# Kernel tuning notes

Hardware: AMD Instinct MI355X
Metric: run time of the kernel (lower is better)

The kernel has to match this reference:

```python
import jax, jax.numpy as jnp
import numpy as np

EPS = 1e-5
GROUPS = 32


def setup_inputs() -> dict:
    key = jax.random.key(0)
    ks = jax.random.split(key, 12)
    b, c, h, w = 8, 256, 64, 64
    s = 1.0 / np.sqrt(c)
    return {
        "x": jax.random.normal(ks[0], (b, c, h, w), jnp.float32),
        "gn_w": jax.random.uniform(ks[1], (c,), jnp.float32, 0.5, 1.5),
        "gn_b": jax.random.normal(ks[2], (c,), jnp.float32) * 0.1,
        "wq": jax.random.normal(ks[3], (c, c), jnp.float32) * s,
        "bq": jax.random.normal(ks[4], (c,), jnp.float32) * 0.02,
        "wk": jax.random.normal(ks[5], (c, c), jnp.float32) * s,
        "bk": jax.random.normal(ks[6], (c,), jnp.float32) * 0.02,
        "wv": jax.random.normal(ks[7], (c, c), jnp.float32) * s,
        "bv": jax.random.normal(ks[8], (c,), jnp.float32) * 0.02,
        "wp": jax.random.normal(ks[9], (c, c), jnp.float32) * s,
        "bp": jax.random.normal(ks[10], (c,), jnp.float32) * 0.02,
        "gamma": jax.random.normal(ks[11], (1,), jnp.float32),
    }


def _group_norm(x, weight, bias):
    b, c, h, w = x.shape
    g = min(c, GROUPS)
    xg = x.reshape(b, g, c // g, h * w)
    mean = xg.mean(axis=(2, 3), keepdims=True)
    var = jnp.var(xg, axis=(2, 3), keepdims=True)
    xn = (xg - mean) * jax.lax.rsqrt(var + EPS)
    xn = xn.reshape(b, c, h, w)
    return xn * weight[None, :, None, None] + bias[None, :, None, None]


def reference(x, gn_w, gn_b, wq, bq, wk, bk, wv, bv, wp, bp, gamma):
    b, c, h, w = x.shape
    x_dash = _group_norm(x, gn_w, gn_b)           # (b,c,h,w)
    xf = x_dash.reshape(b, c, h * w)              # (b,c,n)
    # 1x1 convs == per-pixel linear maps over channels
    q = jnp.einsum('oc,bcn->bon', wq, xf) + bq[None, :, None]
    k = jnp.einsum('oc,bcn->bon', wk, xf) + bk[None, :, None]
    v = jnp.einsum('oc,bcn->bon', wv, xf) + bv[None, :, None]
    # attn[b,i,j] = <q[:,i], k[:,j]> / sqrt(c)
    attn = jnp.einsum('bci,bcj->bij', q, k) / jnp.sqrt(jnp.asarray(c, x.dtype))
    attn = jax.nn.softmax(attn, axis=-1)
    # out[b,c,i] = sum_j v[b,c,j] * attn[b,i,j]
    out = jnp.einsum('bcj,bij->bci', v, attn)
    out = jnp.einsum('oc,bcn->bon', wp, out) + bp[None, :, None]
    out = out.reshape(b, c, h, w)
    return x + gamma[0] * out
```

## Files before the change

kernel.cpp:

```cpp
#include <hip/hip_runtime.h>
#include <cstdint>
#include <cstddef>


#define NB   8
#define NC   256
#define NPIX 4096
#define CPG  8

typedef __attribute__((ext_vector_type(8))) short bf16x8;
typedef __attribute__((ext_vector_type(4))) short s16x4;
typedef __attribute__((ext_vector_type(8))) short s16x8;
typedef __attribute__((ext_vector_type(4))) float f32x4;

__device__ __forceinline__ short f2bf(float f) {
  union { float f; uint32_t u; } v; v.f = f;
  return (short)((v.u + 0x7fffu + ((v.u >> 16) & 1u)) >> 16);
}

__device__ __forceinline__ float bf2f(short s) {
  union { uint32_t u; float f; } v;
  v.u = ((uint32_t)(unsigned short)s) << 16;
  return v.f;
}

__device__ __forceinline__ uint32_t cvtpk_bf(float a, float b) {
  uint32_t r;
  asm("v_cvt_pk_bf16_f32 %0, %1, %2" : "=v"(r) : "v"(a), "v"(b));
  return r;
}

__device__ __forceinline__ f32x4 mfma16(bf16x8 a, bf16x8 b, f32x4 c) {
  return __builtin_amdgcn_mfma_f32_16x16x32_bf16(a, b, c, 0, 0, 0);
}

__device__ __forceinline__ void gload_lds16(const short* g, short* l) {
  __builtin_amdgcn_global_load_lds(
      (const __attribute__((address_space(1))) void*)g,
      (__attribute__((address_space(3))) void*)l, 16, 0, 0);
}

__global__ __launch_bounds__(256) void wconv4(
    const float* __restrict__ w0, const float* __restrict__ w1,
    const float* __restrict__ w2, const float* __restrict__ w3,
    short* __restrict__ o0, short* __restrict__ o1,
    short* __restrict__ o2, short* __restrict__ o3) {
  int m = blockIdx.x >> 6;
  const float* w = (m == 0) ? w0 : (m == 1) ? w1 : (m == 2) ? w2 : w3;
  short* o = (m == 0) ? o0 : (m == 1) ? o1 : (m == 2) ? o2 : o3;
  int i = ((blockIdx.x & 63) * 256 + threadIdx.x) * 4;
  float4 v = *reinterpret_cast<const float4*>(w + i);
  s16x4 p;
  p[0] = f2bf(v.x); p[1] = f2bf(v.y); p[2] = f2bf(v.z); p[3] = f2bf(v.w);
  *reinterpret_cast<s16x4*>(o + i) = p;
}

__global__ __launch_bounds__(1024) void gnorm(const float* __restrict__ x,
                                              const float* __restrict__ gw,
                                              const float* __restrict__ gb,
                                              short* __restrict__ xdt) {
  int b = blockIdx.x >> 5;
  int g = blockIdx.x & 31;
  const float* xp = x + ((size_t)b * NC + (size_t)g * CPG) * NPIX;
  int t = threadIdx.x;

  float s = 0.f, ss = 0.f;
  const float4* xp4 = reinterpret_cast<const float4*>(xp);
  for (int i = t; i < (CPG * NPIX) / 4; i += 1024) {
    float4 v = xp4[i];
    s  += v.x + v.y + v.z + v.w;
    ss += v.x * v.x + v.y * v.y + v.z * v.z + v.w * v.w;
  }
  for (int m = 32; m; m >>= 1) { s += __shfl_xor(s, m); ss += __shfl_xor(ss, m); }
  __shared__ float red[34];
  int wid = t >> 6;
  if ((t & 63) == 0) { red[wid] = s; red[16 + wid] = ss; }
  __syncthreads();
  if (t == 0) {
    float a = 0.f, b2 = 0.f;
    for (int i = 0; i < 16; ++i) { a += red[i]; b2 += red[16 + i]; }
    float mean = a * (1.f / 32768.f);
    float var  = b2 * (1.f / 32768.f) - mean * mean;
    red[32] = mean;
    red[33] = rsqrtf(var + 1e-5f);
  }
  __syncthreads();
  float mean = red[32], rstd = red[33];

  float wv2[CPG], bv2[CPG];
  for (int cc = 0; cc < CPG; ++cc) {
    float wgt = gw[g * CPG + cc] * rstd;
    wv2[cc] = wgt;
    bv2[cc] = gb[g * CPG + cc] - mean * wgt;
  }
  for (int pix = t; pix < NPIX; pix += 1024) {
    s16x8 pk;
    for (int cc = 0; cc < CPG; ++cc)
      pk[cc] = f2bf(fmaf(xp[cc * NPIX + pix], wv2[cc], bv2[cc]));
    *reinterpret_cast<s16x8*>(&xdt[((size_t)b * NPIX + pix) * NC + g * CPG]) = pk;
  }
}

__global__ __launch_bounds__(256) void qkv_gemm(
    const short* __restrict__ wq_bf, const short* __restrict__ wk_bf,
    const short* __restrict__ wv_bf,
    const float* __restrict__ bq, const float* __restrict__ bk,
    const float* __restrict__ bv,
    const short* __restrict__ xdt,
    short* __restrict__ qt, short* __restrict__ kt, short* __restrict__ vv) {
  int nt = blockIdx.x, b = blockIdx.y;

  __shared__ short xtile[64 * 256];
  __shared__ float bias_lds[3][256];
  int t = threadIdx.x;
  const short* xg = xdt + ((size_t)b * NPIX + nt * 64) * NC;
  for (int it = 0; it < 8; ++it) {
    int id = t + it * 256, row = id >> 5, part = id & 31;
    *reinterpret_cast<uint4*>(&xtile[row * 256 + (part ^ (row & 7)) * 8]) =
        *reinterpret_cast<const uint4*>(&xg[(size_t)row * 256 + part * 8]);
  }
  bias_lds[0][t] = bq[t];
  bias_lds[1][t] = bk[t];
  bias_lds[2][t] = bv[t];
  __syncthreads();

  int w = t >> 6, lane = t & 63, g = lane >> 4, lr = lane & 15;
  const short* Ws[3] = {wq_bf, wk_bf, wv_bf};

  for (int mi = 0; mi < 3; ++mi) {
    const short* W = Ws[mi];
    f32x4 acc[4][4];
    f32x4 zz = {0.f, 0.f, 0.f, 0.f};
    for (int i = 0; i < 4; ++i) for (int j = 0; j < 4; ++j) acc[i][j] = zz;

    for (int c0 = 0; c0 < 256; c0 += 32) {
      bf16x8 af[4], bfr[4];
      for (int mf = 0; mf < 4; ++mf)
        af[mf] = *reinterpret_cast<const bf16x8*>(
            &W[(size_t)(w * 64 + mf * 16 + lr) * 256 + c0 + g * 8]);
      for (int nf = 0; nf < 4; ++nf) {
        int row = nf * 16 + lr;
        bfr[nf] = *reinterpret_cast<const bf16x8*>(
            &xtile[row * 256 + (((c0 >> 3) + g) ^ (row & 7)) * 8]);
      }
      for (int mf = 0; mf < 4; ++mf)
        for (int nf = 0; nf < 4; ++nf)
          acc[mf][nf] = mfma16(af[mf], bfr[nf], acc[mf][nf]);
    }

    if (mi < 2) {
      short* outp = (mi == 0) ? qt : kt;
      for (int mf = 0; mf < 4; ++mf)
        for (int nf = 0; nf < 4; ++nf) {
          int ob = w * 64 + mf * 16 + g * 4;
          int n  = nt * 64 + nf * 16 + lr;
          s16x4 pk;
          for (int r = 0; r < 4; ++r)
            pk[r] = f2bf(acc[mf][nf][r] + bias_lds[mi][ob + r]);
          *reinterpret_cast<s16x4*>(&outp[((size_t)b * NPIX + n) * NC + ob]) = pk;
        }
    } else {
      for (int mf = 0; mf < 4; ++mf)
        for (int nf = 0; nf < 4; ++nf) {
          int ob = w * 64 + mf * 16 + g * 4;
          int n  = nt * 64 + nf * 16 + lr;
          for (int r = 0; r < 4; ++r)
            vv[((size_t)b * NC + ob + r) * NPIX + n] =
                f2bf(acc[mf][nf][r] + bias_lds[2][ob + r]);
        }
    }
  }
}

__global__ __launch_bounds__(256, 2) void attn(
    const short* __restrict__ qt, const short* __restrict__ kt,
    const short* __restrict__ vv, short* __restrict__ outp,
    float* __restrict__ lp, int njt, int final_write) {
  int b = blockIdx.x, itile = blockIdx.y, kh = blockIdx.z;
  int jt0 = kh * njt;
  __shared__ short ktile[64 * 256];
  __shared__ short Pb[64 * 64];
  __shared__ float lfin[2][64];

  int t = threadIdx.x, w = t >> 6, lane = t & 63, g = lane >> 4, lr = lane & 15;
  int kk = w >> 1, qq = w & 1;
  int i0 = itile * 64;

  const short* ktg = kt + (size_t)b * NPIX * NC;

  int dmaSrc[8], dmaDst[8];
#pragma unroll
  for (int it = 0; it < 8; ++it) {
    int id = it * 256 + t, row = id >> 5, ch = id & 31;
    dmaSrc[it] = row * 256 + (ch ^ (row & 7)) * 8;
    dmaDst[it] = id * 8;
  }

  {
    const short* kb = ktg + (size_t)jt0 * 16384;
#pragma unroll
    for (int it = 0; it < 8; ++it) gload_lds16(kb + dmaSrc[it], &ktile[dmaDst[it]]);
  }
  const short* kgp = ktg + (size_t)(jt0 + 1) * 16384;

  bf16x8 qf[2][8];
  for (int qi = 0; qi < 2; ++qi) {
    const short* qrow =
        qt + ((size_t)b * NPIX + i0 + 32 * qq + 16 * qi + lr) * NC;
    for (int ks = 0; ks < 8; ++ks)
      qf[qi][ks] = *reinterpret_cast<const bf16x8*>(&qrow[ks * 32 + g * 8]);
  }

  const short* vbase =
      vv + (size_t)b * NC * NPIX + (size_t)(w * 64 + lr) * NPIX + g * 8;

  int row0 = 32 * kk + lr, row1 = row0 + 16;
  int pwo[2][2];
  for (int qi = 0; qi < 2; ++qi) {
    int q_loc = 32 * qq + 16 * qi + lr;
    for (int mt = 0; mt < 2; ++mt)
      pwo[qi][mt] = q_loc * 64 +
                    (((4 * kk + 2 * mt + (g >> 1)) ^ (q_loc & 7)) * 8) +
                    (g & 1) * 4;
  }
  int pr[4][2];
  for (int nf = 0; nf < 4; ++nf)
    for (int ks2 = 0; ks2 < 2; ++ks2) {
      int qc = nf * 16 + lr;
      pr[nf][ks2] = qc * 64 + (((ks2 * 4 + g) ^ (qc & 7)) * 8);
    }

  f32x4 zz = {0.f, 0.f, 0.f, 0.f};
  f32x4 oacc[4][4];
  for (int i = 0; i < 4; ++i) for (int j = 0; j < 4; ++j) oacc[i][j] = zz;
  bf16x8 va0[4], va1[4];
  float l_p[2] = {0.f, 0.f};

  const float sc = 0.0625f, L2E = 1.44269504f;
  const float SCL = sc * L2E;

  for (int j = 0; j < njt; ++j) {
    int jt = jt0 + j;

    asm volatile("s_waitcnt vmcnt(0) lgkmcnt(0)" ::: "memory");
    __builtin_amdgcn_s_barrier();
    asm volatile("" ::: "memory");

    if (j > 0) {
      __builtin_amdgcn_s_setprio(1);
      bf16x8 pb[4];
#pragma unroll
      for (int nf = 0; nf < 4; ++nf)
        pb[nf] = *reinterpret_cast<const bf16x8*>(&Pb[pr[nf][0]]);
#pragma unroll
      for (int mf = 0; mf < 4; ++mf)
#pragma unroll
        for (int nf = 0; nf < 4; ++nf)
          oacc[mf][nf] = mfma16(va0[mf], pb[nf], oacc[mf][nf]);
      __builtin_amdgcn_s_setprio(0);
      const short* vp = vbase + (size_t)(jt - 1) * 64 + 32;
#pragma unroll
      for (int mf = 0; mf < 4; ++mf)
        va1[mf] = *reinterpret_cast<const bf16x8*>(vp + (size_t)mf * (16 * NPIX));
    }

    f32x4 s[2][2];
    s[0][0] = zz; s[0][1] = zz; s[1][0] = zz; s[1][1] = zz;
    __builtin_amdgcn_s_setprio(1);
#pragma unroll
    for (int ks = 0; ks < 8; ++ks) {
      bf16x8 kf0 = *reinterpret_cast<const bf16x8*>(
          &ktile[row0 * 256 + (((ks * 4) + g) ^ (row0 & 7)) * 8]);
      bf16x8 kf1 = *reinterpret_cast<const bf16x8*>(
          &ktile[row1 * 256 + (((ks * 4) + g) ^ (row1 & 7)) * 8]);
      s[0][0] = mfma16(kf0, qf[0][ks], s[0][0]);
      s[0][1] = mfma16(kf0, qf[1][ks], s[0][1]);
      s[1][0] = mfma16(kf1, qf[0][ks], s[1][0]);
      s[1][1] = mfma16(kf1, qf[1][ks], s[1][1]);
    }
    __builtin_amdgcn_s_setprio(0);

    asm volatile("s_waitcnt lgkmcnt(0)" ::: "memory");
    __builtin_amdgcn_s_barrier();
    asm volatile("" ::: "memory");

#pragma unroll
    for (int it = 0; it < 8; ++it)
      gload_lds16(kgp + dmaSrc[it], &ktile[dmaDst[it]]);
    kgp += 16384;

    {
      const short* vp = vbase + (size_t)jt * 64;
#pragma unroll
      for (int mf = 0; mf < 4; ++mf)
        va0[mf] = *reinterpret_cast<const bf16x8*>(vp + (size_t)mf * (16 * NPIX));
    }

    if (j > 0) {
      asm volatile("s_waitcnt vmcnt(12)" ::: "memory");
      __builtin_amdgcn_s_setprio(1);
      bf16x8 pb[4];
#pragma unroll
      for (int nf = 0; nf < 4; ++nf)
        pb[nf] = *reinterpret_cast<const bf16x8*>(&Pb[pr[nf][1]]);
#pragma unroll
      for (int mf = 0; mf < 4; ++mf)
#pragma unroll
        for (int nf = 0; nf < 4; ++nf)
          oacc[mf][nf] = mfma16(va1[mf], pb[nf], oacc[mf][nf]);
      __builtin_amdgcn_s_setprio(0);
    }

    asm volatile("s_waitcnt lgkmcnt(0)" ::: "memory");
    __builtin_amdgcn_s_barrier();
    asm volatile("" ::: "memory");

#pragma unroll
    for (int qi = 0; qi < 2; ++qi) {
      float ps = 0.f;
#pragma unroll
      for (int mt = 0; mt < 2; ++mt) {
        float p0 = exp2f(s[mt][qi][0] * SCL);
        float p1 = exp2f(s[mt][qi][1] * SCL);
        float p2 = exp2f(s[mt][qi][2] * SCL);
        float p3 = exp2f(s[mt][qi][3] * SCL);
        ps += (p0 + p1) + (p2 + p3);
        uint2 pk;
        pk.x = cvtpk_bf(p0, p1);
        pk.y = cvtpk_bf(p2, p3);
        *reinterpret_cast<uint2*>(&Pb[pwo[qi][mt]]) = pk;
      }
      l_p[qi] += ps;
    }
  }

  {
    const short* vp = vbase + (size_t)(jt0 + njt - 1) * 64 + 32;
#pragma unroll
    for (int mf = 0; mf < 4; ++mf)
      va1[mf] = *reinterpret_cast<const bf16x8*>(vp + (size_t)mf * (16 * NPIX));
  }
  asm volatile("s_waitcnt vmcnt(0) lgkmcnt(0)" ::: "memory");
  __builtin_amdgcn_s_barrier();
  asm volatile("" ::: "memory");
  {
    bf16x8 pb[4];
#pragma unroll
    for (int nf = 0; nf < 4; ++nf)
      pb[nf] = *reinterpret_cast<const bf16x8*>(&Pb[pr[nf][0]]);
    for (int mf = 0; mf < 4; ++mf)
      for (int nf = 0; nf < 4; ++nf)
        oacc[mf][nf] = mfma16(va0[mf], pb[nf], oacc[mf][nf]);
#pragma unroll
    for (int nf = 0; nf < 4; ++nf)
      pb[nf] = *reinterpret_cast<const bf16x8*>(&Pb[pr[nf][1]]);
    for (int mf = 0; mf < 4; ++mf)
      for (int nf = 0; nf < 4; ++nf)
        oacc[mf][nf] = mfma16(va1[mf], pb[nf], oacc[mf][nf]);
  }

#pragma unroll
  for (int qi = 0; qi < 2; ++qi) {
    float v = l_p[qi];
    v += __shfl_xor(v, 16);
    v += __shfl_xor(v, 32);
    l_p[qi] = v;
  }
  if (lane < 16) {
    lfin[kk][32 * qq + lr]      = l_p[0];
    lfin[kk][32 * qq + 16 + lr] = l_p[1];
  }
  __syncthreads();

  short* okh = outp + (size_t)kh * NB * NPIX * NC;
  for (int nf = 0; nf < 4; ++nf) {
    int q = nf * 16 + lr;
    float inv = final_write ? 1.f / (lfin[0][q] + lfin[1][q]) : 1.f;
    int i = i0 + q;
    for (int mf = 0; mf < 4; ++mf) {
      int cb = w * 64 + mf * 16 + g * 4;
      s16x4 pk;
      for (int r = 0; r < 4; ++r) pk[r] = f2bf(oacc[mf][nf][r] * inv);
      *reinterpret_cast<s16x4*>(&okh[((size_t)b * NPIX + i) * NC + cb]) = pk;
    }
  }
  if (!final_write && w < 2 && lane < 16) {
    float* lk = lp + (size_t)kh * NB * NPIX + (size_t)b * NPIX + i0;
#pragma unroll
    for (int qi = 0; qi < 2; ++qi) {
      int q = 32 * w + 16 * qi + lane;
      lk[q] = lfin[0][q] + lfin[1][q];
    }
  }
}

__global__ __launch_bounds__(256) void attn_merge(
    const short* __restrict__ o0, const short* __restrict__ o1,
    const float* __restrict__ lp, short* __restrict__ ot) {
  int idx = (blockIdx.x * 256 + threadIdx.x) * 8;
  int row = idx >> 8;
  float inv = 1.f / (lp[row] + lp[NB * NPIX + row]);
  s16x8 a = *reinterpret_cast<const s16x8*>(o0 + idx);
  s16x8 c = *reinterpret_cast<const s16x8*>(o1 + idx);
  s16x8 o;
#pragma unroll
  for (int e = 0; e < 8; ++e)
    o[e] = f2bf((bf2f(a[e]) + bf2f(c[e])) * inv);
  *reinterpret_cast<s16x8*>(ot + idx) = o;
}

__global__ __launch_bounds__(256) void proj_res(
    const short* __restrict__ wp_bf, const float* __restrict__ bp,
    const short* __restrict__ ot, const float* __restrict__ x,
    const float* __restrict__ gamma, float* __restrict__ out) {
  int nt = blockIdx.x, b = blockIdx.y;
  __shared__ short otile[64 * 256];
  __shared__ float bias_lds[256];
  int t = threadIdx.x;
  const short* og = ot + ((size_t)b * NPIX + nt * 64) * NC;
  for (int itx = 0; itx < 8; ++itx) {
    int id = t + itx * 256, row = id >> 5, part = id & 31;
    *reinterpret_cast<uint4*>(&otile[row * 256 + (part ^ (row & 7)) * 8]) =
        *reinterpret_cast<const uint4*>(&og[(size_t)row * 256 + part * 8]);
  }
  bias_lds[t] = bp[t];
  __syncthreads();

  int w = t >> 6, lane = t & 63, g = lane >> 4, lr = lane & 15;
  f32x4 acc[4][4];
  f32x4 zz = {0.f, 0.f, 0.f, 0.f};
  for (int i = 0; i < 4; ++i) for (int j = 0; j < 4; ++j) acc[i][j] = zz;

  for (int c0 = 0; c0 < 256; c0 += 32) {
    bf16x8 af[4], bfr[4];
    for (int mf = 0; mf < 4; ++mf)
      af[mf] = *reinterpret_cast<const bf16x8*>(
          &wp_bf[(size_t)(w * 64 + mf * 16 + lr) * 256 + c0 + g * 8]);
    for (int nf = 0; nf < 4; ++nf) {
      int row = nf * 16 + lr;
      bfr[nf] = *reinterpret_cast<const bf16x8*>(
          &otile[row * 256 + (((c0 >> 3) + g) ^ (row & 7)) * 8]);
    }
    for (int mf = 0; mf < 4; ++mf)
      for (int nf = 0; nf < 4; ++nf)
        acc[mf][nf] = mfma16(af[mf], bfr[nf], acc[mf][nf]);
  }

  float gm = gamma[0];
  for (int mf = 0; mf < 4; ++mf)
    for (int nf = 0; nf < 4; ++nf) {
      int ob = w * 64 + mf * 16 + g * 4;
      int n  = nt * 64 + nf * 16 + lr;
      for (int r = 0; r < 4; ++r) {
        size_t idx = ((size_t)b * NC + ob + r) * NPIX + n;
        out[idx] = x[idx] + gm * (acc[mf][nf][r] + bias_lds[ob + r]);
      }
    }
}

extern "C" void kernel_launch(void* const* d_in, const int* in_sizes, int n_in,
                              void* d_out, int out_size, void* d_ws, size_t ws_size,
                              hipStream_t stream) {
  (void)in_sizes; (void)n_in; (void)out_size;
  const float* x     = (const float*)d_in[0];
  const float* gn_w  = (const float*)d_in[1];
  const float* gn_b  = (const float*)d_in[2];
  const float* wq    = (const float*)d_in[3];
  const float* bq    = (const float*)d_in[4];
  const float* wk    = (const float*)d_in[5];
  const float* bk    = (const float*)d_in[6];
  const float* wv    = (const float*)d_in[7];
  const float* bv    = (const float*)d_in[8];
  const float* wp    = (const float*)d_in[9];
  const float* bp    = (const float*)d_in[10];
  const float* gamma = (const float*)d_in[11];
  float* out = (float*)d_out;

  char* ws = (char*)d_ws;
  const size_t WSZ = 131072;
  const size_t TSZ = (size_t)NB * NPIX * NC * 2;
  short* wq_bf = (short*)(ws);
  short* wk_bf = (short*)(ws + WSZ);
  short* wv_bf = (short*)(ws + 2 * WSZ);
  short* wp_bf = (short*)(ws + 3 * WSZ);
  short* xdt   = (short*)(ws + 4 * WSZ);
  short* qt    = (short*)(ws + 4 * WSZ + TSZ);
  short* kt    = (short*)(ws + 4 * WSZ + 2 * TSZ);
  short* vv    = (short*)(ws + 4 * WSZ + 3 * TSZ);
  short* ot    = xdt;
  short* opart = (short*)(ws + 4 * WSZ + 4 * TSZ);
  float* lpb   = (float*)(ws + 4 * WSZ + 6 * TSZ);
  const size_t NEED = 4 * WSZ + 6 * TSZ + (size_t)2 * NB * NPIX * sizeof(float);

  wconv4<<<256, 256, 0, stream>>>(wq, wk, wv, wp, wq_bf, wk_bf, wv_bf, wp_bf);

  gnorm<<<256, 1024, 0, stream>>>(x, gn_w, gn_b, xdt);

  qkv_gemm<<<dim3(64, 8), 256, 0, stream>>>(wq_bf, wk_bf, wv_bf, bq, bk, bv,
                                            xdt, qt, kt, vv);

  if (ws_size >= NEED) {
    attn<<<dim3(8, 64, 2), 256, 0, stream>>>(qt, kt, vv, opart, lpb, 32, 0);
    attn_merge<<<4096, 256, 0, stream>>>(opart, opart + (size_t)NB * NPIX * NC,
                                         lpb, ot);
  } else {
    attn<<<dim3(8, 64, 1), 256, 0, stream>>>(qt, kt, vv, ot, lpb, 64, 1);
  }

  proj_res<<<dim3(64, 8), 256, 0, stream>>>(wp_bf, bp, ot, x, gamma, out);
}
```

Baseline: 289.8 us.

## Halve attention key tile to 32 rows and double-buffer the P tile

The attention kernel now processes 32-key tiles instead of 64, with each wave computing one 16-row score fragment, and the probability tile is double-buffered in LDS so the previous tile's PV MFMAs read one buffer while new probabilities go to the other. This drops one barrier per iteration and the split V half-loads, and it shrinks LDS use, which may allow more resident blocks. In exchange there are twice as many loop iterations, each with less MFMA work to hide the barrier and DMA latency.

```diff
diff --git a/kernel.cpp b/kernel.cpp
--- a/kernel.cpp
+++ b/kernel.cpp
@@ -178,8 +178,8 @@
     float* __restrict__ lp, int njt, int final_write) {
   int b = blockIdx.x, itile = blockIdx.y, kh = blockIdx.z;
   int jt0 = kh * njt;
-  __shared__ short ktile[64 * 256];
-  __shared__ short Pb[64 * 64];
+  __shared__ short ktile[32 * 256];
+  __shared__ short Pb[2][64 * 32];
   __shared__ float lfin[2][64];
 
   int t = threadIdx.x, w = t >> 6, lane = t & 63, g = lane >> 4, lr = lane & 15;
@@ -188,20 +188,16 @@
 
   const short* ktg = kt + (size_t)b * NPIX * NC;
 
-  int dmaSrc[8], dmaDst[8];
-#pragma unroll
-  for (int it = 0; it < 8; ++it) {
-    int id = it * 256 + t, row = id >> 5, ch = id & 31;
-    dmaSrc[it] = row * 256 + (ch ^ (row & 7)) * 8;
-    dmaDst[it] = id * 8;
-  }
+  int dsrc = (t >> 5) * 256 + ((t & 31) ^ ((t >> 5) & 7)) * 8;
+  int ddst = t * 8;
 
   {
-    const short* kb = ktg + (size_t)jt0 * 16384;
-#pragma unroll
-    for (int it = 0; it < 8; ++it) gload_lds16(kb + dmaSrc[it], &ktile[dmaDst[it]]);
-  }
-  const short* kgp = ktg + (size_t)(jt0 + 1) * 16384;
+    const short* kb = ktg + (size_t)jt0 * 8192;
+#pragma unroll
+    for (int it = 0; it < 4; ++it)
+      gload_lds16(kb + it * 2048 + dsrc, &ktile[it * 2048 + ddst]);
+  }
+  const short* kgp = ktg + (size_t)(jt0 + 1) * 8192;
 
   bf16x8 qf[2][8];
   for (int qi = 0; qi < 2; ++qi) {
@@ -214,26 +210,23 @@
   const short* vbase =
       vv + (size_t)b * NC * NPIX + (size_t)(w * 64 + lr) * NPIX + g * 8;
 
-  int row0 = 32 * kk + lr, row1 = row0 + 16;
-  int pwo[2][2];
+  int krow = 16 * kk + lr;
+  int pwo[2];
   for (int qi = 0; qi < 2; ++qi) {
     int q_loc = 32 * qq + 16 * qi + lr;
-    for (int mt = 0; mt < 2; ++mt)
-      pwo[qi][mt] = q_loc * 64 +
-                    (((4 * kk + 2 * mt + (g >> 1)) ^ (q_loc & 7)) * 8) +
-                    (g & 1) * 4;
-  }
-  int pr[4][2];
-  for (int nf = 0; nf < 4; ++nf)
-    for (int ks2 = 0; ks2 < 2; ++ks2) {
-      int qc = nf * 16 + lr;
-      pr[nf][ks2] = qc * 64 + (((ks2 * 4 + g) ^ (qc & 7)) * 8);
-    }
+    pwo[qi] = q_loc * 32 + (((2 * kk + (g >> 1)) ^ (q_loc & 3)) * 8) +
+              (g & 1) * 4;
+  }
+  int pr[4];
+  for (int nf = 0; nf < 4; ++nf) {
+    int qc = nf * 16 + lr;
+    pr[nf] = qc * 32 + ((g ^ (qc & 3)) * 8);
+  }
 
   f32x4 zz = {0.f, 0.f, 0.f, 0.f};
   f32x4 oacc[4][4];
   for (int i = 0; i < 4; ++i) for (int j = 0; j < 4; ++j) oacc[i][j] = zz;
-  bf16x8 va0[4], va1[4];
+  bf16x8 va[4];
   float l_p[2] = {0.f, 0.f};
 
   const float sc = 0.0625f, L2E = 1.44269504f;
@@ -241,6 +234,7 @@
 
   for (int j = 0; j < njt; ++j) {
     int jt = jt0 + j;
+    int cur = j & 1, prv = cur ^ 1;
 
     asm volatile("s_waitcnt vmcnt(0) lgkmcnt(0)" ::: "memory");
     __builtin_amdgcn_s_barrier();
@@ -251,32 +245,23 @@
       bf16x8 pb[4];
 #pragma unroll
       for (int nf = 0; nf < 4; ++nf)
-        pb[nf] = *reinterpret_cast<const bf16x8*>(&Pb[pr[nf][0]]);
+        pb[nf] = *reinterpret_cast<const bf16x8*>(&Pb[prv][pr[nf]]);
 #pragma unroll
       for (int mf = 0; mf < 4; ++mf)
 #pragma unroll
         for (int nf = 0; nf < 4; ++nf)
-          oacc[mf][nf] = mfma16(va0[mf], pb[nf], oacc[mf][nf]);
+          oacc[mf][nf] = mfma16(va[mf], pb[nf], oacc[mf][nf]);
       __builtin_amdgcn_s_setprio(0);
-      const short* vp = vbase + (size_t)(jt - 1) * 64 + 32;
-#pragma unroll
-      for (int mf = 0; mf < 4; ++mf)
-        va1[mf] = *reinterpret_cast<const bf16x8*>(vp + (size_t)mf * (16 * NPIX));
-    }
-
-    f32x4 s[2][2];
-    s[0][0] = zz; s[0][1] = zz; s[1][0] = zz; s[1][1] = zz;
+    }
+
+    f32x4 s0 = zz, s1 = zz;
     __builtin_amdgcn_s_setprio(1);
 #pragma unroll
     for (int ks = 0; ks < 8; ++ks) {
-      bf16x8 kf0 = *reinterpret_cast<const bf16x8*>(
-          &ktile[row0 * 256 + (((ks * 4) + g) ^ (row0 & 7)) * 8]);
-      bf16x8 kf1 = *reinterpret_cast<const bf16x8*>(
-          &ktile[row1 * 256 + (((ks * 4) + g) ^ (row1 & 7)) * 8]);
-      s[0][0] = mfma16(kf0, qf[0][ks], s[0][0]);
-      s[0][1] = mfma16(kf0, qf[1][ks], s[0][1]);
-      s[1][0] = mfma16(kf1, qf[0][ks], s[1][0]);
-      s[1][1] = mfma16(kf1, qf[1][ks], s[1][1]);
+      bf16x8 kf = *reinterpret_cast<const bf16x8*>(
+          &ktile[krow * 256 + (((ks * 4) + g) ^ (lr & 7)) * 8]);
+      s0 = mfma16(kf, qf[0][ks], s0);
+      s1 = mfma16(kf, qf[1][ks], s1);
     }
     __builtin_amdgcn_s_setprio(0);
 
@@ -285,61 +270,31 @@
     asm volatile("" ::: "memory");
 
 #pragma unroll
-    for (int it = 0; it < 8; ++it)
-      gload_lds16(kgp + dmaSrc[it], &ktile[dmaDst[it]]);
-    kgp += 16384;
+    for (int it = 0; it < 4; ++it)
+      gload_lds16(kgp + it * 2048 + dsrc, &ktile[it * 2048 + ddst]);
+    kgp += 8192;
 
     {
-      const short* vp = vbase + (size_t)jt * 64;
-#pragma unroll
-      for (int mf = 0; mf < 4; ++mf)
-        va0[mf] = *reinterpret_cast<const bf16x8*>(vp + (size_t)mf * (16 * NPIX));
-    }
-
-    if (j > 0) {
-      asm volatile("s_waitcnt vmcnt(12)" ::: "memory");
-      __builtin_amdgcn_s_setprio(1);
-      bf16x8 pb[4];
-#pragma unroll
-      for (int nf = 0; nf < 4; ++nf)
-        pb[nf] = *reinterpret_cast<const bf16x8*>(&Pb[pr[nf][1]]);
-#pragma unroll
-      for (int mf = 0; mf < 4; ++mf)
-#pragma unroll
-        for (int nf = 0; nf < 4; ++nf)
-          oacc[mf][nf] = mfma16(va1[mf], pb[nf], oacc[mf][nf]);
-      __builtin_amdgcn_s_setprio(0);
-    }
-
-    asm volatile("s_waitcnt lgkmcnt(0)" ::: "memory");
-    __builtin_amdgcn_s_barrier();
-    asm volatile("" ::: "memory");
-
-#pragma unroll
-    for (int qi = 0; qi < 2; ++qi) {
-      float ps = 0.f;
-#pragma unroll
-      for (int mt = 0; mt < 2; ++mt) {
-        float p0 = exp2f(s[mt][qi][0] * SCL);
-        float p1 = exp2f(s[mt][qi][1] * SCL);
-        float p2 = exp2f(s[mt][qi][2] * SCL);
-        float p3 = exp2f(s[mt][qi][3] * SCL);
-        ps += (p0 + p1) + (p2 + p3);
-        uint2 pk;
-        pk.x = cvtpk_bf(p0, p1);
-        pk.y = cvtpk_bf(p2, p3);
-        *reinterpret_cast<uint2*>(&Pb[pwo[qi][mt]]) = pk;
-      }
-      l_p[qi] += ps;
-    }
-  }
-
-  {
-    const short* vp = vbase + (size_t)(jt0 + njt - 1) * 64 + 32;
-#pragma unroll
-    for (int mf = 0; mf < 4; ++mf)
-      va1[mf] = *reinterpret_cast<const bf16x8*>(vp + (size_t)mf * (16 * NPIX));
-  }
+      const short* vp = vbase + (size_t)jt * 32;
+#pragma unroll
+      for (int mf = 0; mf < 4; ++mf)
+        va[mf] = *reinterpret_cast<const bf16x8*>(vp + (size_t)mf * (16 * NPIX));
+    }
+
+    {
+      float p0 = exp2f(s0[0] * SCL), p1 = exp2f(s0[1] * SCL);
+      float p2 = exp2f(s0[2] * SCL), p3 = exp2f(s0[3] * SCL);
+      l_p[0] += (p0 + p1) + (p2 + p3);
+      uint2 pk; pk.x = cvtpk_bf(p0, p1); pk.y = cvtpk_bf(p2, p3);
+      *reinterpret_cast<uint2*>(&Pb[cur][pwo[0]]) = pk;
+      p0 = exp2f(s1[0] * SCL); p1 = exp2f(s1[1] * SCL);
+      p2 = exp2f(s1[2] * SCL); p3 = exp2f(s1[3] * SCL);
+      l_p[1] += (p0 + p1) + (p2 + p3);
+      pk.x = cvtpk_bf(p0, p1); pk.y = cvtpk_bf(p2, p3);
+      *reinterpret_cast<uint2*>(&Pb[cur][pwo[1]]) = pk;
+    }
+  }
+
   asm volatile("s_waitcnt vmcnt(0) lgkmcnt(0)" ::: "memory");
   __builtin_amdgcn_s_barrier();
   asm volatile("" ::: "memory");
@@ -347,16 +302,10 @@
     bf16x8 pb[4];
 #pragma unroll
     for (int nf = 0; nf < 4; ++nf)
-      pb[nf] = *reinterpret_cast<const bf16x8*>(&Pb[pr[nf][0]]);
+      pb[nf] = *reinterpret_cast<const bf16x8*>(&Pb[1][pr[nf]]);
     for (int mf = 0; mf < 4; ++mf)
       for (int nf = 0; nf < 4; ++nf)
-        oacc[mf][nf] = mfma16(va0[mf], pb[nf], oacc[mf][nf]);
-#pragma unroll
-    for (int nf = 0; nf < 4; ++nf)
-      pb[nf] = *reinterpret_cast<const bf16x8*>(&Pb[pr[nf][1]]);
-    for (int mf = 0; mf < 4; ++mf)
-      for (int nf = 0; nf < 4; ++nf)
-        oacc[mf][nf] = mfma16(va1[mf], pb[nf], oacc[mf][nf]);
+        oacc[mf][nf] = mfma16(va[mf], pb[nf], oacc[mf][nf]);
   }
 
 #pragma unroll
@@ -500,11 +449,11 @@
                                             xdt, qt, kt, vv);
 
   if (ws_size >= NEED) {
-    attn<<<dim3(8, 64, 2), 256, 0, stream>>>(qt, kt, vv, opart, lpb, 32, 0);
+    attn<<<dim3(8, 64, 2), 256, 0, stream>>>(qt, kt, vv, opart, lpb, 64, 0);
     attn_merge<<<4096, 256, 0, stream>>>(opart, opart + (size_t)NB * NPIX * NC,
                                          lpb, ot);
   } else {
-    attn<<<dim3(8, 64, 1), 256, 0, stream>>>(qt, kt, vv, ot, lpb, 64, 1);
+    attn<<<dim3(8, 64, 1), 256, 0, stream>>>(qt, kt, vv, ot, lpb, 128, 1);
   }
 
   proj_res<<<dim3(64, 8), 256, 0, stream>>>(wp_bf, bp, ot, x, gamma, out);
```

Result: no change. 285.8 us (-1.4%).
